# Kernel optimization log

Hardware: AMD Instinct MI355X
Metric: run time of the kernel (lower is better)

The kernel has to match this reference:

```python
import jax, jax.numpy as jnp
import numpy as np

B, N, IN_DIM, OUT_DIM = 8, 2048, 768, 768


def setup_inputs() -> dict:
    key = jax.random.key(0)
    ks = jax.random.split(key, 9)
    s_in = 1.0 / np.sqrt(IN_DIM)
    return {
        "x": jax.random.normal(ks[0], (B, N, IN_DIM), dtype=jnp.float32),
        "ln_gamma": jnp.ones((IN_DIM,), dtype=jnp.float32),
        "ln_beta": jnp.zeros((IN_DIM,), dtype=jnp.float32),
        "wq": jax.random.uniform(ks[1], (OUT_DIM, IN_DIM), jnp.float32, -s_in, s_in),
        "bq": jax.random.uniform(ks[2], (OUT_DIM,), jnp.float32, -s_in, s_in),
        "wk": jax.random.uniform(ks[3], (OUT_DIM, IN_DIM), jnp.float32, -s_in, s_in),
        "bk": jax.random.uniform(ks[4], (OUT_DIM,), jnp.float32, -s_in, s_in),
        "wv": jax.random.uniform(ks[5], (OUT_DIM, IN_DIM), jnp.float32, -s_in, s_in),
        "bv": jax.random.uniform(ks[6], (OUT_DIM,), jnp.float32, -s_in, s_in),
    }


def reference(x, ln_gamma, ln_beta, wq, bq, wk, bk, wv, bv):
    # LayerNorm over last dim (eps matches torch default 1e-5)
    mu = jnp.mean(x, axis=-1, keepdims=True)
    var = jnp.mean(jnp.square(x - mu), axis=-1, keepdims=True)
    xn = (x - mu) * jax.lax.rsqrt(var + 1e-5) * ln_gamma + ln_beta
    # QKV projections (torch Linear: y = x W^T + b)
    q = jnp.einsum('bnd,od->bno', xn, wq) + bq
    k = jnp.einsum('bnd,od->bno', xn, wk) + bk
    v = jnp.einsum('bnd,od->bno', xn, wv) + bv
    # unscaled attention, as in source (no 1/sqrt(d) scaling)
    scores = jnp.einsum('bqo,bko->bqk', q, k)  # [B, N, N]
    attn = jax.nn.softmax(scores, axis=2)
    # torch.dropout(x, 0.5, False) with train=False is a no-op
    return jnp.einsum('bqk,bko->bqo', attn, v)
```

## Files before the change

### kernel.cpp

```cpp
#include <hip/hip_runtime.h>

#define NB 8
#define SEQ 2048
#define DIM 768

typedef _Float16 f16;
typedef _Float16 f16x8 __attribute__((ext_vector_type(8)));
typedef _Float16 f16x4 __attribute__((ext_vector_type(4)));
typedef short s16x8 __attribute__((ext_vector_type(8)));
typedef unsigned short u16x4 __attribute__((ext_vector_type(4)));
typedef float f32x4 __attribute__((ext_vector_type(4)));

typedef __attribute__((address_space(1))) void as1_void;
typedef __attribute__((address_space(3))) void as3_void;

__device__ __forceinline__ void gld16(const void* g, void* l) {
  __builtin_amdgcn_global_load_lds((as1_void*)g, (as3_void*)l, 16, 0, 0);
}

__device__ __forceinline__ unsigned short f2b(float f) {
  unsigned int u = __builtin_bit_cast(unsigned int, f);
  u += 0x7FFFu + ((u >> 16) & 1u);
  return (unsigned short)(u >> 16);
}
__device__ __forceinline__ float b2f(unsigned short b) {
  unsigned int u = ((unsigned int)b) << 16;
  return __builtin_bit_cast(float, u);
}

#define EXP_SHIFT 46.0f

__global__ __launch_bounds__(256) void ln_kernel(const float* __restrict__ x,
                                                 const float* __restrict__ gamma,
                                                 const float* __restrict__ beta,
                                                 f16* __restrict__ xn) {
  const int row = blockIdx.x;
  const int t = threadIdx.x;
  const float* xr = x + (size_t)row * DIM;
  float v0 = xr[t], v1 = xr[t + 256], v2 = xr[t + 512];
  float s = v0 + v1 + v2;
  float s2 = v0 * v0 + v1 * v1 + v2 * v2;
#pragma unroll
  for (int o = 32; o > 0; o >>= 1) {
    s += __shfl_down(s, o);
    s2 += __shfl_down(s2, o);
  }
  __shared__ float red[8];
  const int w = t >> 6;
  if ((t & 63) == 0) { red[w] = s; red[4 + w] = s2; }
  __syncthreads();
  s = red[0] + red[1] + red[2] + red[3];
  s2 = red[4] + red[5] + red[6] + red[7];
  const float mu = s * (1.0f / DIM);
  const float var = s2 * (1.0f / DIM) - mu * mu;
  const float inv = rsqrtf(var + 1e-5f);
  f16* xo = xn + (size_t)row * DIM;
  xo[t]       = (f16)((v0 - mu) * inv * gamma[t]       + beta[t]);
  xo[t + 256] = (f16)((v1 - mu) * inv * gamma[t + 256] + beta[t + 256]);
  xo[t + 512] = (f16)((v2 - mu) * inv * gamma[t + 512] + beta[t + 512]);
}

__global__ __launch_bounds__(256) void cvt_w_kernel(const float* __restrict__ wq,
                                                    const float* __restrict__ wk,
                                                    const float* __restrict__ wv,
                                                    f16* __restrict__ wcat) {
  const int i = (blockIdx.x * 256 + threadIdx.x) * 4;
  const int per = DIM * DIM;
  const float* src;
  int rem;
  if (i < per) { src = wq; rem = i; }
  else if (i < 2 * per) { src = wk; rem = i - per; }
  else { src = wv; rem = i - 2 * per; }
  float4 v = *(const float4*)(src + rem);
  f16x4 o;
  o[0] = (f16)v.x; o[1] = (f16)v.y; o[2] = (f16)v.z; o[3] = (f16)v.w;
  *(f16x4*)(wcat + i) = o;
}

template <int MODE>
__global__ __launch_bounds__(256, 4) void gemm_s(const f16* __restrict__ Abase,
                                                 const f16* __restrict__ Bbase,
                                                 void* __restrict__ Out0,
                                                 void* __restrict__ Out1,
                                                 void* __restrict__ Out2,
                                                 const float* __restrict__ bias0,
                                                 const float* __restrict__ bias1,
                                                 const float* __restrict__ bias2,
                                                 int Kdim) {
  const int tid = threadIdx.x;
  const int lane = tid & 63;
  const int w = tid >> 6;
  const int wr = w >> 1, wc = w & 1;

  const int nwg = gridDim.x;
  const int fb = blockIdx.x;
  const int v = (fb & 7) * (nwg >> 3) + (fb >> 3);

  int bm, z, bncol;
  const f16 *Ap, *Bp;
  size_t lda, ldb;
  if constexpr (MODE == 0) {
    const int m = v / 18, u = v % 18;
    z = u / 6; bncol = (u % 6) * 128; bm = m * 128;
    Ap = Abase + (size_t)bm * DIM;                              lda = DIM;
    Bp = Bbase + (size_t)z * DIM * DIM + (size_t)bncol * DIM;   ldb = DIM;
  } else if constexpr (MODE == 1) {
    z = v >> 8; const int r = v & 255;
    bm = (r >> 4) * 128; bncol = (r & 15) * 128;
    Ap = Abase + (size_t)z * SEQ * DIM + (size_t)bm * DIM;      lda = DIM;
    Bp = Bbase + (size_t)z * SEQ * DIM + (size_t)bncol * DIM;   ldb = DIM;
  } else {
    z = v / 96; const int r = v % 96;
    bm = (r / 6) * 128; bncol = (r % 6) * 128;
    Ap = Abase + (size_t)z * SEQ * SEQ + (size_t)bm * SEQ;      lda = SEQ;
    Bp = Bbase + (size_t)z * DIM * SEQ + (size_t)bncol * SEQ;   ldb = SEQ;
  }
  const int K = Kdim;

  __shared__ __align__(16) f16 As[128 * 64];
  __shared__ __align__(16) f16 Bs[128 * 64];

  const int srow = w * 8 + (lane >> 3);
  const int sslot = (lane & 7) ^ (lane >> 3);
  const f16* ga = Ap + (size_t)srow * lda + sslot * 8;
  const f16* gb = Bp + (size_t)srow * ldb + sslot * 8;

  f32x4 acc[4][4];
#pragma unroll
  for (int i = 0; i < 4; i++)
#pragma unroll
    for (int j = 0; j < 4; j++) acc[i][j] = (f32x4){0.f, 0.f, 0.f, 0.f};

  const int g4 = lane >> 4;
  const int rx = lane & 7;

  const int nk = K >> 6;
  for (int kt = 0; kt < nk; ++kt) {
    const size_t k0 = (size_t)kt << 6;
    __syncthreads();
#pragma unroll
    for (int i = 0; i < 4; i++) {
      gld16(ga + (size_t)(i * 32) * lda + k0, &As[(i * 32 + w * 8) * 64]);
      gld16(gb + (size_t)(i * 32) * ldb + k0, &Bs[(i * 32 + w * 8) * 64]);
    }
    __builtin_amdgcn_s_waitcnt(0);
    __syncthreads();
#pragma unroll
    for (int ks = 0; ks < 2; ++ks) {
      const int sl = ((ks * 4 + g4) ^ rx) * 8;
      f16x8 af[4], bf[4];
#pragma unroll
      for (int i = 0; i < 4; i++)
        af[i] = *(const f16x8*)(&As[(wr * 64 + i * 16 + (lane & 15)) * 64 + sl]);
#pragma unroll
      for (int j = 0; j < 4; j++)
        bf[j] = *(const f16x8*)(&Bs[(wc * 64 + j * 16 + (lane & 15)) * 64 + sl]);
#pragma unroll
      for (int i = 0; i < 4; i++)
#pragma unroll
        for (int j = 0; j < 4; j++) {
          if constexpr (MODE == 2)
            acc[i][j] = __builtin_amdgcn_mfma_f32_16x16x32_bf16(
                __builtin_bit_cast(s16x8, af[i]), __builtin_bit_cast(s16x8, bf[j]),
                acc[i][j], 0, 0, 0);
          else
            acc[i][j] = __builtin_amdgcn_mfma_f32_16x16x32_f16(af[i], bf[j], acc[i][j], 0, 0, 0);
        }
    }
  }

  const int lrow = (lane >> 4) * 4;
  const int lcol = lane & 15;

  if constexpr (MODE == 0) {
    const float* bias = (z == 0) ? bias0 : (z == 1) ? bias1 : bias2;
    if (z < 2) {
      f16* Oz = (f16*)((z == 0) ? Out0 : Out1);
#pragma unroll
      for (int j = 0; j < 4; j++) {
        const int gc = bncol + wc * 64 + j * 16 + lcol;
        const float bb = bias[gc];
#pragma unroll
        for (int i = 0; i < 4; i++) {
          const int grow = bm + wr * 64 + i * 16 + lrow;
          f16* o = Oz + (size_t)grow * DIM + gc;
          o[0 * DIM] = (f16)(acc[i][j][0] + bb);
          o[1 * DIM] = (f16)(acc[i][j][1] + bb);
          o[2 * DIM] = (f16)(acc[i][j][2] + bb);
          o[3 * DIM] = (f16)(acc[i][j][3] + bb);
        }
      }
    } else {
      unsigned short* Vt = (unsigned short*)Out2;
#pragma unroll
      for (int j = 0; j < 4; j++) {
        const int gc = bncol + wc * 64 + j * 16 + lcol;
        const float bb = bias[gc];
#pragma unroll
        for (int i = 0; i < 4; i++) {
          const int grow = bm + wr * 64 + i * 16 + lrow;
          const int bidx = grow >> 11, nt = grow & (SEQ - 1);
          u16x4 pk;
          pk[0] = f2b(acc[i][j][0] + bb);
          pk[1] = f2b(acc[i][j][1] + bb);
          pk[2] = f2b(acc[i][j][2] + bb);
          pk[3] = f2b(acc[i][j][3] + bb);
          *(u16x4*)(Vt + ((size_t)bidx * DIM + gc) * SEQ + nt) = pk;
        }
      }
    }
  } else if constexpr (MODE == 1) {
    unsigned short* Oz = (unsigned short*)Out0 + (size_t)z * SEQ * SEQ;
    float* lsum = (float*)Out1;
    float rs[4][4];
#pragma unroll
    for (int i = 0; i < 4; i++)
#pragma unroll
      for (int r = 0; r < 4; r++) rs[i][r] = 0.f;
#pragma unroll
    for (int j = 0; j < 4; j++) {
      const int gc = bncol + wc * 64 + j * 16 + lcol;
#pragma unroll
      for (int i = 0; i < 4; i++) {
        const int grow = bm + wr * 64 + i * 16 + lrow;
        unsigned short* o = Oz + (size_t)grow * SEQ + gc;
#pragma unroll
        for (int r = 0; r < 4; r++) {
          const unsigned short eb = f2b(__expf(acc[i][j][r] - EXP_SHIFT));
          o[(size_t)r * SEQ] = eb;
          rs[i][r] += b2f(eb);
        }
      }
    }
#pragma unroll
    for (int i = 0; i < 4; i++)
#pragma unroll
      for (int r = 0; r < 4; r++) {
        float s = rs[i][r];
        s += __shfl_xor(s, 1);
        s += __shfl_xor(s, 2);
        s += __shfl_xor(s, 4);
        s += __shfl_xor(s, 8);
        if ((lane & 15) == 0)
          atomicAdd(lsum + (size_t)z * SEQ + bm + wr * 64 + i * 16 + lrow + r, s);
      }
  } else {
    const float* lsum = bias0;
    float invl[4][4];
#pragma unroll
    for (int i = 0; i < 4; i++)
#pragma unroll
      for (int r = 0; r < 4; r++)
        invl[i][r] = 1.0f / lsum[(size_t)z * SEQ + bm + wr * 64 + i * 16 + lrow + r];
    float* Oz = (float*)Out0 + (size_t)z * SEQ * DIM;
#pragma unroll
    for (int j = 0; j < 4; j++) {
      const int gc = bncol + wc * 64 + j * 16 + lcol;
#pragma unroll
      for (int i = 0; i < 4; i++) {
        const int grow = bm + wr * 64 + i * 16 + lrow;
        float* o = Oz + (size_t)grow * DIM + gc;
        o[0 * DIM] = acc[i][j][0] * invl[i][0];
        o[1 * DIM] = acc[i][j][1] * invl[i][1];
        o[2 * DIM] = acc[i][j][2] * invl[i][2];
        o[3 * DIM] = acc[i][j][3] * invl[i][3];
      }
    }
  }
}

extern "C" void kernel_launch(void* const* d_in, const int* in_sizes, int n_in,
                              void* d_out, int out_size, void* d_ws, size_t ws_size,
                              hipStream_t stream) {
  (void)in_sizes; (void)n_in; (void)out_size;
  const float* x  = (const float*)d_in[0];
  const float* lg = (const float*)d_in[1];
  const float* lb = (const float*)d_in[2];
  const float* wq = (const float*)d_in[3];
  const float* bq = (const float*)d_in[4];
  const float* wk = (const float*)d_in[5];
  const float* bk = (const float*)d_in[6];
  const float* wv = (const float*)d_in[7];
  const float* bv = (const float*)d_in[8];
  float* out = (float*)d_out;

  const size_t MT = (size_t)NB * SEQ;
  f16* xn  = (f16*)d_ws;
  f16* wc  = xn + MT * DIM;
  f16* Q   = wc + (size_t)3 * DIM * DIM;
  f16* Km  = Q + MT * DIM;
  unsigned short* Vt = (unsigned short*)(Km + MT * DIM);
  char* dyn = (char*)(Vt + MT * DIM);
  const size_t used = (size_t)(dyn - (char*)d_ws);
  const size_t per_batch = (size_t)SEQ * SEQ * 2 + (size_t)SEQ * 4;
  size_t rem = (ws_size > used) ? (ws_size - used) : 0;
  int nbc = (int)(rem / per_batch);
  if (nbc < 1) nbc = 1;
  if (nbc > NB) nbc = NB;
  unsigned short* E = (unsigned short*)dyn;
  float* lsum = (float*)(dyn + (size_t)nbc * SEQ * SEQ * 2);

  cvt_w_kernel<<<dim3(3 * DIM * DIM / 1024), 256, 0, stream>>>(wq, wk, wv, wc);
  ln_kernel<<<dim3((unsigned)MT), 256, 0, stream>>>(x, lg, lb, xn);
  gemm_s<0><<<dim3(128 * 18), 256, 0, stream>>>(xn, wc, Q, Km, Vt, bq, bk, bv, DIM);

  for (int b0 = 0; b0 < NB; b0 += nbc) {
    const int nb = (NB - b0 < nbc) ? (NB - b0) : nbc;
    hipMemsetAsync(lsum, 0, (size_t)nb * SEQ * 4, stream);
    gemm_s<1><<<dim3(nb * 256), 256, 0, stream>>>(
        Q + (size_t)b0 * SEQ * DIM, Km + (size_t)b0 * SEQ * DIM,
        E, lsum, nullptr, nullptr, nullptr, nullptr, DIM);
    gemm_s<2><<<dim3(nb * 96), 256, 0, stream>>>(
        (const f16*)E, (const f16*)(Vt + (size_t)b0 * DIM * SEQ),
        out + (size_t)b0 * SEQ * DIM, nullptr, nullptr, lsum, nullptr, nullptr, SEQ);
  }
}
```

Baseline: 230.1 us.

## Fold Q projection into K via precomputed Wq^T Wk, eliminating Q GEMM

Rewrites the scores as xn·(Wq^T Wk)·xn^T plus rank-one bias terms. Wq^T Wk is precomputed once per call by a small GEMM, and the per-row bias terms are computed inside the LayerNorm kernel. The projection GEMM now produces only K' and V, which removes a third of its work and the Q writeback, and the score GEMM reads xn directly. The trade is extra small kernels (transpose, bias vectors, 768^3 GEMM) and fp16 rounding of the fused weight matrix, which could change accuracy because the attention is unscaled.

```diff
diff --git a/kernel.cpp b/kernel.cpp
--- a/kernel.cpp
+++ b/kernel.cpp
@@ -30,10 +30,105 @@
 
 #define EXP_SHIFT 46.0f
 
+__global__ __launch_bounds__(256) void tr_kernel(const float* __restrict__ wq,
+                                                 const float* __restrict__ wk,
+                                                 f16* __restrict__ wqT,
+                                                 f16* __restrict__ wkT) {
+  const int t = threadIdx.x;
+  const int id = blockIdx.x;
+  const int zz = id / 36, r = id % 36;
+  const int br = (r / 6) * 128;
+  const int bc = (r % 6) * 128;
+  const float* src = zz ? wk : wq;
+  f16* dst = zz ? wkT : wqT;
+  __shared__ f16 tile[128][132];
+#pragma unroll
+  for (int c = 0; c < 16; c++) {
+    const int row = c * 8 + (t >> 5);
+    const int col = (t & 31) * 4;
+    float4 v = *(const float4*)(src + (size_t)(br + row) * DIM + bc + col);
+    tile[col + 0][row] = (f16)v.x;
+    tile[col + 1][row] = (f16)v.y;
+    tile[col + 2][row] = (f16)v.z;
+    tile[col + 3][row] = (f16)v.w;
+  }
+  __syncthreads();
+#pragma unroll
+  for (int c = 0; c < 16; c++) {
+    const int drow = c * 8 + (t >> 5);
+    const int dcol = (t & 31) * 4;
+    f16x4 o;
+    o[0] = tile[drow][dcol + 0];
+    o[1] = tile[drow][dcol + 1];
+    o[2] = tile[drow][dcol + 2];
+    o[3] = tile[drow][dcol + 3];
+    *(f16x4*)(dst + (size_t)(bc + drow) * DIM + br + dcol) = o;
+  }
+}
+
+__global__ __launch_bounds__(256) void uwc_kernel(const f16* __restrict__ wqT,
+                                                  const f16* __restrict__ wkT,
+                                                  const float* __restrict__ bq,
+                                                  const float* __restrict__ bk,
+                                                  float* __restrict__ u,
+                                                  float* __restrict__ w,
+                                                  float* __restrict__ cbuf) {
+  const int b = blockIdx.x;
+  const int t = threadIdx.x;
+  const int lane = t & 63, wvi = t >> 6;
+  if (b == 24) {
+    if (wvi == 0) {
+      float ss = 0.f;
+      for (int i = lane; i < DIM; i += 64) ss += bq[i] * bk[i];
+#pragma unroll
+      for (int o = 32; o; o >>= 1) ss += __shfl_down(ss, o);
+      if (lane == 0) *cbuf = ss;
+    }
+    return;
+  }
+  const f16* Ms = (b < 12) ? wqT : wkT;
+  const float* vec = (b < 12) ? bk : bq;
+  float* dst = (b < 12) ? u : w;
+  const int rbase = (b % 12) * 64 + wvi * 16;
+  float va[8], vb[4];
+#pragma unroll
+  for (int e = 0; e < 8; e++) va[e] = vec[lane * 8 + e];
+#pragma unroll
+  for (int e = 0; e < 4; e++) vb[e] = vec[512 + lane * 4 + e];
+  for (int rr = 0; rr < 16; rr++) {
+    const int d = rbase + rr;
+    const f16* row = Ms + (size_t)d * DIM;
+    f16x8 a = *(const f16x8*)(row + lane * 8);
+    f16x4 b4 = *(const f16x4*)(row + 512 + lane * 4);
+    float ss = 0.f;
+#pragma unroll
+    for (int e = 0; e < 8; e++) ss += (float)a[e] * va[e];
+#pragma unroll
+    for (int e = 0; e < 4; e++) ss += (float)b4[e] * vb[e];
+#pragma unroll
+    for (int o = 32; o; o >>= 1) ss += __shfl_down(ss, o);
+    if (lane == 0) dst[d] = ss;
+  }
+}
+
+__global__ __launch_bounds__(256) void cvt_wv_kernel(const float* __restrict__ src,
+                                                     f16* __restrict__ dst) {
+  const int i = (blockIdx.x * 256 + threadIdx.x) * 4;
+  float4 v = *(const float4*)(src + i);
+  f16x4 o;
+  o[0] = (f16)v.x; o[1] = (f16)v.y; o[2] = (f16)v.z; o[3] = (f16)v.w;
+  *(f16x4*)(dst + i) = o;
+}
+
 __global__ __launch_bounds__(256) void ln_kernel(const float* __restrict__ x,
                                                  const float* __restrict__ gamma,
                                                  const float* __restrict__ beta,
-                                                 f16* __restrict__ xn) {
+                                                 const float* __restrict__ u,
+                                                 const float* __restrict__ w,
+                                                 const float* __restrict__ cbuf,
+                                                 f16* __restrict__ xn,
+                                                 float* __restrict__ rvec,
+                                                 float* __restrict__ svec) {
   const int row = blockIdx.x;
   const int t = threadIdx.x;
   const float* xr = x + (size_t)row * DIM;
@@ -46,35 +141,33 @@
     s2 += __shfl_down(s2, o);
   }
   __shared__ float red[8];
-  const int w = t >> 6;
-  if ((t & 63) == 0) { red[w] = s; red[4 + w] = s2; }
+  const int wv = t >> 6;
+  if ((t & 63) == 0) { red[wv] = s; red[4 + wv] = s2; }
   __syncthreads();
   s = red[0] + red[1] + red[2] + red[3];
   s2 = red[4] + red[5] + red[6] + red[7];
   const float mu = s * (1.0f / DIM);
   const float var = s2 * (1.0f / DIM) - mu * mu;
   const float inv = rsqrtf(var + 1e-5f);
+  const float y0 = (v0 - mu) * inv * gamma[t] + beta[t];
+  const float y1 = (v1 - mu) * inv * gamma[t + 256] + beta[t + 256];
+  const float y2 = (v2 - mu) * inv * gamma[t + 512] + beta[t + 512];
   f16* xo = xn + (size_t)row * DIM;
-  xo[t]       = (f16)((v0 - mu) * inv * gamma[t]       + beta[t]);
-  xo[t + 256] = (f16)((v1 - mu) * inv * gamma[t + 256] + beta[t + 256]);
-  xo[t + 512] = (f16)((v2 - mu) * inv * gamma[t + 512] + beta[t + 512]);
-}
-
-__global__ __launch_bounds__(256) void cvt_w_kernel(const float* __restrict__ wq,
-                                                    const float* __restrict__ wk,
-                                                    const float* __restrict__ wv,
-                                                    f16* __restrict__ wcat) {
-  const int i = (blockIdx.x * 256 + threadIdx.x) * 4;
-  const int per = DIM * DIM;
-  const float* src;
-  int rem;
-  if (i < per) { src = wq; rem = i; }
-  else if (i < 2 * per) { src = wk; rem = i - per; }
-  else { src = wv; rem = i - 2 * per; }
-  float4 v = *(const float4*)(src + rem);
-  f16x4 o;
-  o[0] = (f16)v.x; o[1] = (f16)v.y; o[2] = (f16)v.z; o[3] = (f16)v.w;
-  *(f16x4*)(wcat + i) = o;
+  xo[t] = (f16)y0; xo[t + 256] = (f16)y1; xo[t + 512] = (f16)y2;
+  float rp = u[t] * y0 + u[t + 256] * y1 + u[t + 512] * y2;
+  float sp = w[t] * y0 + w[t + 256] * y1 + w[t + 512] * y2;
+#pragma unroll
+  for (int o = 32; o > 0; o >>= 1) {
+    rp += __shfl_down(rp, o);
+    sp += __shfl_down(sp, o);
+  }
+  __syncthreads();
+  if ((t & 63) == 0) { red[wv] = rp; red[4 + wv] = sp; }
+  __syncthreads();
+  if (t == 0) {
+    rvec[row] = red[0] + red[1] + red[2] + red[3] + cbuf[0];
+    svec[row] = red[4] + red[5] + red[6] + red[7];
+  }
 }
 
 template <int MODE>
@@ -94,14 +187,14 @@
 
   const int nwg = gridDim.x;
   const int fb = blockIdx.x;
-  const int v = (fb & 7) * (nwg >> 3) + (fb >> 3);
+  const int v = (MODE == 3) ? fb : ((fb & 7) * (nwg >> 3) + (fb >> 3));
 
   int bm, z, bncol;
   const f16 *Ap, *Bp;
   size_t lda, ldb;
   if constexpr (MODE == 0) {
-    const int m = v / 18, u = v % 18;
-    z = u / 6; bncol = (u % 6) * 128; bm = m * 128;
+    const int m = v / 12, q12 = v % 12;
+    z = q12 / 6; bncol = (q12 % 6) * 128; bm = m * 128;
     Ap = Abase + (size_t)bm * DIM;                              lda = DIM;
     Bp = Bbase + (size_t)z * DIM * DIM + (size_t)bncol * DIM;   ldb = DIM;
   } else if constexpr (MODE == 1) {
@@ -109,11 +202,16 @@
     bm = (r >> 4) * 128; bncol = (r & 15) * 128;
     Ap = Abase + (size_t)z * SEQ * DIM + (size_t)bm * DIM;      lda = DIM;
     Bp = Bbase + (size_t)z * SEQ * DIM + (size_t)bncol * DIM;   ldb = DIM;
-  } else {
+  } else if constexpr (MODE == 2) {
     z = v / 96; const int r = v % 96;
     bm = (r / 6) * 128; bncol = (r % 6) * 128;
     Ap = Abase + (size_t)z * SEQ * SEQ + (size_t)bm * SEQ;      lda = SEQ;
     Bp = Bbase + (size_t)z * DIM * SEQ + (size_t)bncol * SEQ;   ldb = SEQ;
+  } else {
+    const int m = v / 6, n = v % 6;
+    z = 0; bm = m * 128; bncol = n * 128;
+    Ap = Abase + (size_t)bm * DIM;                              lda = DIM;
+    Bp = Bbase + (size_t)bncol * DIM;                           ldb = DIM;
   }
   const int K = Kdim;
 
@@ -173,21 +271,19 @@
   const int lcol = lane & 15;
 
   if constexpr (MODE == 0) {
-    const float* bias = (z == 0) ? bias0 : (z == 1) ? bias1 : bias2;
-    if (z < 2) {
-      f16* Oz = (f16*)((z == 0) ? Out0 : Out1);
+    if (z == 0) {
+      f16* Oz = (f16*)Out0;
 #pragma unroll
       for (int j = 0; j < 4; j++) {
         const int gc = bncol + wc * 64 + j * 16 + lcol;
-        const float bb = bias[gc];
 #pragma unroll
         for (int i = 0; i < 4; i++) {
           const int grow = bm + wr * 64 + i * 16 + lrow;
           f16* o = Oz + (size_t)grow * DIM + gc;
-          o[0 * DIM] = (f16)(acc[i][j][0] + bb);
-          o[1 * DIM] = (f16)(acc[i][j][1] + bb);
-          o[2 * DIM] = (f16)(acc[i][j][2] + bb);
-          o[3 * DIM] = (f16)(acc[i][j][3] + bb);
+          o[0 * DIM] = (f16)acc[i][j][0];
+          o[1 * DIM] = (f16)acc[i][j][1];
+          o[2 * DIM] = (f16)acc[i][j][2];
+          o[3 * DIM] = (f16)acc[i][j][3];
         }
       }
     } else {
@@ -195,7 +291,7 @@
 #pragma unroll
       for (int j = 0; j < 4; j++) {
         const int gc = bncol + wc * 64 + j * 16 + lcol;
-        const float bb = bias[gc];
+        const float bb = bias2[gc];
 #pragma unroll
         for (int i = 0; i < 4; i++) {
           const int grow = bm + wr * 64 + i * 16 + lrow;
@@ -212,6 +308,12 @@
   } else if constexpr (MODE == 1) {
     unsigned short* Oz = (unsigned short*)Out0 + (size_t)z * SEQ * SEQ;
     float* lsum = (float*)Out1;
+    float r16[4][4];
+#pragma unroll
+    for (int i = 0; i < 4; i++)
+#pragma unroll
+      for (int r = 0; r < 4; r++)
+        r16[i][r] = bias1[(size_t)z * SEQ + bm + wr * 64 + i * 16 + lrow + r];
     float rs[4][4];
 #pragma unroll
     for (int i = 0; i < 4; i++)
@@ -220,13 +322,14 @@
 #pragma unroll
     for (int j = 0; j < 4; j++) {
       const int gc = bncol + wc * 64 + j * 16 + lcol;
+      const float sc = bias2[(size_t)z * SEQ + gc];
 #pragma unroll
       for (int i = 0; i < 4; i++) {
         const int grow = bm + wr * 64 + i * 16 + lrow;
         unsigned short* o = Oz + (size_t)grow * SEQ + gc;
 #pragma unroll
         for (int r = 0; r < 4; r++) {
-          const unsigned short eb = f2b(__expf(acc[i][j][r] - EXP_SHIFT));
+          const unsigned short eb = f2b(__expf(acc[i][j][r] + r16[i][r] + sc - EXP_SHIFT));
           o[(size_t)r * SEQ] = eb;
           rs[i][r] += b2f(eb);
         }
@@ -244,7 +347,7 @@
         if ((lane & 15) == 0)
           atomicAdd(lsum + (size_t)z * SEQ + bm + wr * 64 + i * 16 + lrow + r, s);
       }
-  } else {
+  } else if constexpr (MODE == 2) {
     const float* lsum = bias0;
     float invl[4][4];
 #pragma unroll
@@ -264,6 +367,21 @@
         o[1 * DIM] = acc[i][j][1] * invl[i][1];
         o[2 * DIM] = acc[i][j][2] * invl[i][2];
         o[3 * DIM] = acc[i][j][3] * invl[i][3];
+      }
+    }
+  } else {
+    f16* Oz = (f16*)Out0;
+#pragma unroll
+    for (int j = 0; j < 4; j++) {
+      const int gc = bncol + wc * 64 + j * 16 + lcol;
+#pragma unroll
+      for (int i = 0; i < 4; i++) {
+        const int grow = bm + wr * 64 + i * 16 + lrow;
+        f16* o = Oz + (size_t)grow * DIM + gc;
+        o[0 * DIM] = (f16)acc[i][j][0];
+        o[1 * DIM] = (f16)acc[i][j][1];
+        o[2 * DIM] = (f16)acc[i][j][2];
+        o[3 * DIM] = (f16)acc[i][j][3];
       }
     }
   }
@@ -286,11 +404,17 @@
 
   const size_t MT = (size_t)NB * SEQ;
   f16* xn  = (f16*)d_ws;
-  f16* wc  = xn + MT * DIM;
-  f16* Q   = wc + (size_t)3 * DIM * DIM;
-  f16* Km  = Q + MT * DIM;
-  unsigned short* Vt = (unsigned short*)(Km + MT * DIM);
-  char* dyn = (char*)(Vt + MT * DIM);
+  f16* wcb = xn + MT * DIM;
+  f16* wqT = wcb + (size_t)2 * DIM * DIM;
+  f16* wkT = wqT + (size_t)DIM * DIM;
+  f16* Kt  = wkT + (size_t)DIM * DIM;
+  unsigned short* Vt = (unsigned short*)(Kt + MT * DIM);
+  float* uv  = (float*)(Vt + MT * DIM);
+  float* wv2 = uv + DIM;
+  float* cb  = wv2 + DIM;
+  float* rv  = cb + 4;
+  float* sv  = rv + MT;
+  char* dyn = (char*)(sv + MT);
   const size_t used = (size_t)(dyn - (char*)d_ws);
   const size_t per_batch = (size_t)SEQ * SEQ * 2 + (size_t)SEQ * 4;
   size_t rem = (ws_size > used) ? (ws_size - used) : 0;
@@ -300,16 +424,21 @@
   unsigned short* E = (unsigned short*)dyn;
   float* lsum = (float*)(dyn + (size_t)nbc * SEQ * SEQ * 2);
 
-  cvt_w_kernel<<<dim3(3 * DIM * DIM / 1024), 256, 0, stream>>>(wq, wk, wv, wc);
-  ln_kernel<<<dim3((unsigned)MT), 256, 0, stream>>>(x, lg, lb, xn);
-  gemm_s<0><<<dim3(128 * 18), 256, 0, stream>>>(xn, wc, Q, Km, Vt, bq, bk, bv, DIM);
+  tr_kernel<<<dim3(72), 256, 0, stream>>>(wq, wk, wqT, wkT);
+  uwc_kernel<<<dim3(25), 256, 0, stream>>>(wqT, wkT, bq, bk, uv, wv2, cb);
+  cvt_wv_kernel<<<dim3(576), 256, 0, stream>>>(wv, wcb + (size_t)DIM * DIM);
+  gemm_s<3><<<dim3(36), 256, 0, stream>>>(wqT, wkT, wcb, nullptr, nullptr,
+                                          nullptr, nullptr, nullptr, DIM);
+  ln_kernel<<<dim3((unsigned)MT), 256, 0, stream>>>(x, lg, lb, uv, wv2, cb, xn, rv, sv);
+  gemm_s<0><<<dim3(128 * 12), 256, 0, stream>>>(xn, wcb, Kt, nullptr, Vt,
+                                                nullptr, nullptr, bv, DIM);
 
   for (int b0 = 0; b0 < NB; b0 += nbc) {
     const int nb = (NB - b0 < nbc) ? (NB - b0) : nbc;
     hipMemsetAsync(lsum, 0, (size_t)nb * SEQ * 4, stream);
     gemm_s<1><<<dim3(nb * 256), 256, 0, stream>>>(
-        Q + (size_t)b0 * SEQ * DIM, Km + (size_t)b0 * SEQ * DIM,
-        E, lsum, nullptr, nullptr, nullptr, nullptr, DIM);
+        xn + (size_t)b0 * SEQ * DIM, Kt + (size_t)b0 * SEQ * DIM,
+        E, lsum, nullptr, nullptr, rv + (size_t)b0 * SEQ, sv + (size_t)b0 * SEQ, DIM);
     gemm_s<2><<<dim3(nb * 96), 256, 0, stream>>>(
         (const f16*)E, (const f16*)(Vt + (size_t)b0 * DIM * SEQ),
         out + (size_t)b0 * SEQ * DIM, nullptr, nullptr, lsum, nullptr, nullptr, SEQ);
```

Result: slower. 276.3 us (+20.1%).
